# Performance work log

Hardware: AMD Instinct MI355X
Metric: run time of the kernel (lower is better)

The kernel has to match this reference:

```python
import jax, jax.numpy as jnp
import numpy as np

B, CK, CQ, CV, CO, H, W = 4, 256, 256, 256, 64, 24, 24


def setup_inputs() -> dict:
    key = jax.random.key(0)
    ks = jax.random.split(key, 9)
    s = lambda k, shape, fan: jax.random.normal(k, shape, jnp.float32) * (fan ** -0.5)
    return {
        "key": jax.random.normal(ks[0], (B, CK, H, W), jnp.float32),
        "query": jax.random.normal(ks[1], (B, CQ, H, W), jnp.float32),
        "value": jax.random.normal(ks[2], (B, CV, H, W), jnp.float32),
        "Wk": s(ks[3], (CO, CK), CK),   # 1x1 conv weight for key transform
        "bk": jnp.zeros((CO,), jnp.float32),
        "Wq": s(ks[4], (CO, CQ), CQ),   # 1x1 conv weight for query transform
        "bq": jnp.zeros((CO,), jnp.float32),
        "wf": s(ks[5], (CO,), CO),      # channel-flattening 1x1 conv (CO -> 1)
        "bf": jnp.zeros((), jnp.float32),
    }


def reference(key, query, value, Wk, bk, Wq, bq, wf, bf):
    b, _, hq, wq = query.shape
    nk = key.shape[2] * key.shape[3]
    nq = hq * wq
    # 1x1 conv == per-pixel linear; flatten spatial to (B, N, CO)
    k_ = jnp.einsum('bchw,oc->bhwo', key, Wk).reshape(b, nk, -1) + bk
    q_ = jnp.einsum('bchw,oc->bhwo', query, Wq).reshape(b, nq, -1) + bq
    # broadcast add: (B, Nk, 1, CO) + (B, 1, Nq, CO) -> tanh -> reduce channels
    pre = jnp.tanh(k_[:, :, None, :] + q_[:, None, :, :])
    scores = jnp.einsum('bkqc,c->bkq', pre, wf) + bf
    attn = jax.nn.sigmoid(scores)                      # (B, Nk, Nq)
    v_ = value.reshape(b, value.shape[1], nk)          # (B, CV, Nk)
    out = jnp.einsum('bkq,bck->bcq', attn, v_)         # (B, CV, Nq)
    return out.reshape(b, value.shape[1], hq, wq)
```

## Files before the change

kernel.cpp:

```cpp
#include <hip/hip_runtime.h>
#include <hip/hip_bf16.h>

#define BB 4
#define CIN 256
#define CO 64
#define NN 576
#define NKC 18
#define NQT 36

typedef __attribute__((ext_vector_type(8))) short short8;
typedef __attribute__((ext_vector_type(4))) float floatx4;

__device__ __forceinline__ unsigned short f2bf(float f) {
    unsigned int u = __float_as_uint(f);
    unsigned int r = (u + 0x7fffu + ((u >> 16) & 1u)) >> 16;
    return (unsigned short)r;
}

__global__ void __launch_bounds__(256) proj_exp_fused(
    const float* __restrict__ key, const float* __restrict__ query,
    const float* __restrict__ Wk, const float* __restrict__ Wq,
    const float* __restrict__ bk, const float* __restrict__ bq,
    float* __restrict__ ek, float* __restrict__ eq)
{
    int nt16 = blockIdx.x;
    int b    = blockIdx.y;
    int z    = blockIdx.z;
    const float* src  = z ? query : key;
    const float* W    = z ? Wq : Wk;
    const float* bias = z ? bq : bk;
    float*       outp = z ? eq : ek;

    __shared__ float tile[256 * 17];

    int t = threadIdx.x, l = t & 63, w = t >> 6;

    const float* sbase = src + (size_t)b * CIN * NN + (size_t)nt16 * 16;
    #pragma unroll
    for (int i = 0; i < 4; ++i) {
        int f4  = t + i * 256;
        int c   = f4 >> 2;
        int col = (f4 & 3) * 4;
        float4 v = *(const float4*)(sbase + (size_t)c * NN + col);
        float* d = &tile[c * 17 + col];
        d[0] = v.x; d[1] = v.y; d[2] = v.z; d[3] = v.w;
    }
    __syncthreads();

    int nt = w;
    int m  = l & 15;
    int o  = nt * 16 + (l & 15);
    floatx4 acc = {0.f, 0.f, 0.f, 0.f};
    #pragma unroll
    for (int kc = 0; kc < 8; ++kc) {
        int cb = kc * 32 + (l >> 4) * 8;
        short8 a;
        #pragma unroll
        for (int j = 0; j < 8; ++j)
            a[j] = (short)f2bf(tile[(cb + j) * 17 + m]);
        const float4* p = (const float4*)(W + (size_t)o * CIN + cb);
        float4 v0 = p[0], v1 = p[1];
        short8 bfr;
        bfr[0] = (short)f2bf(v0.x); bfr[1] = (short)f2bf(v0.y);
        bfr[2] = (short)f2bf(v0.z); bfr[3] = (short)f2bf(v0.w);
        bfr[4] = (short)f2bf(v1.x); bfr[5] = (short)f2bf(v1.y);
        bfr[6] = (short)f2bf(v1.z); bfr[7] = (short)f2bf(v1.w);
        acc = __builtin_amdgcn_mfma_f32_16x16x32_bf16(a, bfr, acc, 0, 0, 0);
    }

    int n0 = nt16 * 16;
    float bv = bias[o];
    #pragma unroll
    for (int rr = 0; rr < 4; ++rr) {
        int row = (l >> 4) * 4 + rr;
        outp[((size_t)b * NN + n0 + row) * CO + o] = __expf(2.0f * (acc[rr] + bv));
    }
}

__global__ void __launch_bounds__(256, 3) attn_pack_kernel(
    const float* __restrict__ ek, const float* __restrict__ eq,
    const float* __restrict__ wf, const float* __restrict__ bfp,
    unsigned short* __restrict__ Bp)
{
    int b  = blockIdx.z;
    int k0 = blockIdx.y * 32;
    int q0 = blockIdx.x * 64;
    int t  = threadIdx.x;
    int l  = t & 63;
    int w  = __builtin_amdgcn_readfirstlane(t >> 6);

    __shared__ float eqs[64 * 65];
    __shared__ float sc[32 * 65];

    const float4* esrc = (const float4*)(eq + ((size_t)b * NN + q0) * CO);
    #pragma unroll
    for (int i = 0; i < 4; ++i) {
        int f4  = t + i * 256;
        int row = f4 >> 4, c4 = (f4 & 15) * 4;
        float4 v = esrc[f4];
        int a = row * 65 + c4;
        eqs[a + 0] = v.x; eqs[a + 1] = v.y; eqs[a + 2] = v.z; eqs[a + 3] = v.w;
    }

    float4 w2v[16];
    float C = bfp[0];
    const float4* wfp4 = (const float4*)wf;
    #pragma unroll
    for (int i = 0; i < 16; ++i) {
        float4 wv = wfp4[i];
        C += wv.x + wv.y + wv.z + wv.w;
        wv.x *= 2.0f; wv.y *= 2.0f; wv.z *= 2.0f; wv.w *= 2.0f;
        w2v[i] = wv;
    }
    __syncthreads();

    float4 eqv[16];
    #pragma unroll
    for (int i = 0; i < 16; ++i) {
        int a = l * 65 + i * 4;
        eqv[i].x = eqs[a]; eqv[i].y = eqs[a + 1];
        eqv[i].z = eqs[a + 2]; eqv[i].w = eqs[a + 3];
    }

    #pragma unroll 1
    for (int kk = 0; kk < 8; ++kk) {
        int k = k0 + w * 8 + kk;
        const float4* ekr = (const float4*)(ek + ((size_t)b * NN + k) * CO);
        float a0 = 0.f, a1 = 0.f, a2 = 0.f, a3 = 0.f;
        #pragma unroll
        for (int i = 0; i < 16; ++i) {
            float4 k4 = ekr[i];
            float4 e4 = eqv[i];
            float4 w4 = w2v[i];
            a0 = fmaf(w4.x, __builtin_amdgcn_rcpf(fmaf(k4.x, e4.x, 1.0f)), a0);
            a1 = fmaf(w4.y, __builtin_amdgcn_rcpf(fmaf(k4.y, e4.y, 1.0f)), a1);
            a2 = fmaf(w4.z, __builtin_amdgcn_rcpf(fmaf(k4.z, e4.z, 1.0f)), a2);
            a3 = fmaf(w4.w, __builtin_amdgcn_rcpf(fmaf(k4.w, e4.w, 1.0f)), a3);
        }
        float score = C - (a0 + a1) - (a2 + a3);
        float sg = __builtin_amdgcn_rcpf(1.0f + __expf(-score));
        sc[(w * 8 + kk) * 65 + l] = sg;
    }
    __syncthreads();

    int col = w * 16 + (l & 15);
    int row = (l >> 4) * 8;
    uint4 o;
    o.x = (unsigned)f2bf(sc[(row + 0) * 65 + col]) | ((unsigned)f2bf(sc[(row + 1) * 65 + col]) << 16);
    o.y = (unsigned)f2bf(sc[(row + 2) * 65 + col]) | ((unsigned)f2bf(sc[(row + 3) * 65 + col]) << 16);
    o.z = (unsigned)f2bf(sc[(row + 4) * 65 + col]) | ((unsigned)f2bf(sc[(row + 5) * 65 + col]) << 16);
    o.w = (unsigned)f2bf(sc[(row + 6) * 65 + col]) | ((unsigned)f2bf(sc[(row + 7) * 65 + col]) << 16);
    size_t qt = (size_t)blockIdx.x * 4 + w;
    *(uint4*)(Bp + (((size_t)b * NQT + qt) * NKC + blockIdx.y) * 512 + l * 8) = o;
}

__global__ void __launch_bounds__(256) av_mfma_kernel(
    const float* __restrict__ value,
    const unsigned short* __restrict__ Bp,
    float* __restrict__ out)
{
    int b  = blockIdx.z;
    int ct = blockIdx.y;
    int qx = blockIdx.x;
    int t  = threadIdx.x;
    int l  = t & 63;
    int w  = __builtin_amdgcn_readfirstlane(t >> 6);

    floatx4 acc[4] = {{0.f,0.f,0.f,0.f},{0.f,0.f,0.f,0.f},
                      {0.f,0.f,0.f,0.f},{0.f,0.f,0.f,0.f}};

    const float* vb = value + ((size_t)b * CIN + ct * 16 + (l & 15)) * NN + (l >> 4) * 8;
    const unsigned short* bbase = Bp + ((size_t)b * NQT + (size_t)qx * 4) * NKC * 512 + l * 8;

    for (int kc = w; kc < NKC; kc += 4) {
        const float4* p = (const float4*)(vb + kc * 32);
        float4 v0 = p[0], v1 = p[1];
        short8 a;
        a[0] = (short)f2bf(v0.x); a[1] = (short)f2bf(v0.y);
        a[2] = (short)f2bf(v0.z); a[3] = (short)f2bf(v0.w);
        a[4] = (short)f2bf(v1.x); a[5] = (short)f2bf(v1.y);
        a[6] = (short)f2bf(v1.z); a[7] = (short)f2bf(v1.w);
        #pragma unroll
        for (int qt = 0; qt < 4; ++qt) {
            short8 bq = *(const short8*)(bbase + ((size_t)qt * NKC + kc) * 512);
            acc[qt] = __builtin_amdgcn_mfma_f32_16x16x32_bf16(a, bq, acc[qt], 0, 0, 0);
        }
    }

    __shared__ float red[4][64][17];
    #pragma unroll
    for (int qt = 0; qt < 4; ++qt)
        #pragma unroll
        for (int r = 0; r < 4; ++r)
            red[w][l][qt * 4 + r] = acc[qt][r];
    __syncthreads();

    int q = qx * 64 + w * 16 + (l & 15);
    #pragma unroll
    for (int r = 0; r < 4; ++r) {
        float s = red[0][l][w * 4 + r] + red[1][l][w * 4 + r]
                + red[2][l][w * 4 + r] + red[3][l][w * 4 + r];
        int c = ct * 16 + (l >> 4) * 4 + r;
        out[((size_t)b * CIN + c) * NN + q] = s;
    }
}

extern "C" void kernel_launch(void* const* d_in, const int* in_sizes, int n_in,
                              void* d_out, int out_size, void* d_ws, size_t ws_size,
                              hipStream_t stream) {
    const float* key   = (const float*)d_in[0];
    const float* query = (const float*)d_in[1];
    const float* value = (const float*)d_in[2];
    const float* Wk    = (const float*)d_in[3];
    const float* bk    = (const float*)d_in[4];
    const float* Wq    = (const float*)d_in[5];
    const float* bq    = (const float*)d_in[6];
    const float* wf    = (const float*)d_in[7];
    const float* bf    = (const float*)d_in[8];
    float* out = (float*)d_out;

    float* ws = (float*)d_ws;
    float* ek = ws;
    float* eq = ek + (size_t)BB * NN * CO;
    unsigned short* Bp = (unsigned short*)(eq + (size_t)BB * NN * CO);

    dim3 gp(NN / 16, BB, 2);
    proj_exp_fused<<<gp, 256, 0, stream>>>(key, query, Wk, Wq, bk, bq, ek, eq);

    dim3 ga(NN / 64, NN / 32, BB);
    attn_pack_kernel<<<ga, 256, 0, stream>>>(ek, eq, wf, bf, Bp);

    dim3 gm(NN / 64, 16, BB);
    av_mfma_kernel<<<gm, 256, 0, stream>>>(value, Bp, out);
}
```

Before: 102.9 us.

## Fuse all stages into one cooperative kernel with grid syncs and prepack V

Replaces three separate launches with a single cooperative kernel of 648 blocks that runs projection, attention scoring and AV matmul as stages separated by grid.sync, and falls back to separate kernels if the cooperative launch fails. It also adds a stage that converts value to bf16 in MFMA fragment layout alongside the projection, so the AV stage loads packed fragments instead of converting fp32 on the fly. The goal is to remove launch gaps and redundant per-block conversions. The costs are grid-barrier overhead, occupancy limits needed for co-residency, and extra workspace traffic for the packed V.

```diff
diff --git a/kernel.cpp b/kernel.cpp
--- a/kernel.cpp
+++ b/kernel.cpp
@@ -1,5 +1,7 @@
 #include <hip/hip_runtime.h>
-#include <hip/hip_bf16.h>
+#include <hip/hip_cooperative_groups.h>
+
+namespace cg = cooperative_groups;
 
 #define BB 4
 #define CIN 256
@@ -17,23 +19,19 @@
     return (unsigned short)r;
 }
 
-__global__ void __launch_bounds__(256) proj_exp_fused(
+__device__ __forceinline__ void stage_proj(
+    int z, int b, int nt16, int t,
     const float* __restrict__ key, const float* __restrict__ query,
     const float* __restrict__ Wk, const float* __restrict__ Wq,
     const float* __restrict__ bk, const float* __restrict__ bq,
-    float* __restrict__ ek, float* __restrict__ eq)
-{
-    int nt16 = blockIdx.x;
-    int b    = blockIdx.y;
-    int z    = blockIdx.z;
+    float* __restrict__ ek, float* __restrict__ eq,
+    float* tile )
+{
+    int l = t & 63, w = t >> 6;
     const float* src  = z ? query : key;
     const float* W    = z ? Wq : Wk;
     const float* bias = z ? bq : bk;
     float*       outp = z ? eq : ek;
-
-    __shared__ float tile[256 * 17];
-
-    int t = threadIdx.x, l = t & 63, w = t >> 6;
 
     const float* sbase = src + (size_t)b * CIN * NN + (size_t)nt16 * 16;
     #pragma unroll
@@ -47,9 +45,8 @@
     }
     __syncthreads();
 
-    int nt = w;
-    int m  = l & 15;
-    int o  = nt * 16 + (l & 15);
+    int m = l & 15;
+    int o = w * 16 + (l & 15);
     floatx4 acc = {0.f, 0.f, 0.f, 0.f};
     #pragma unroll
     for (int kc = 0; kc < 8; ++kc) {
@@ -77,20 +74,37 @@
     }
 }
 
-__global__ void __launch_bounds__(256, 3) attn_pack_kernel(
+__device__ __forceinline__ void stage_vpack(
+    int funit, int l, const float* __restrict__ value,
+    unsigned short* __restrict__ Vp)
+{
+    int b  = funit / 288;
+    int r  = funit % 288;
+    int ct = r / 18;
+    int kc = r % 18;
+    int c = ct * 16 + (l & 15);
+    int k = kc * 32 + (l >> 4) * 8;
+    const float4* p = (const float4*)(value + ((size_t)b * CIN + c) * NN + k);
+    float4 v0 = p[0], v1 = p[1];
+    uint4 u;
+    u.x = (unsigned)f2bf(v0.x) | ((unsigned)f2bf(v0.y) << 16);
+    u.y = (unsigned)f2bf(v0.z) | ((unsigned)f2bf(v0.w) << 16);
+    u.z = (unsigned)f2bf(v1.x) | ((unsigned)f2bf(v1.y) << 16);
+    u.w = (unsigned)f2bf(v1.z) | ((unsigned)f2bf(v1.w) << 16);
+    *(uint4*)(Vp + (((size_t)b * 16 + ct) * NKC + kc) * 512 + l * 8) = u;
+}
+
+__device__ __forceinline__ void stage_attn(
+    int b, int ky, int qx, int t,
     const float* __restrict__ ek, const float* __restrict__ eq,
     const float* __restrict__ wf, const float* __restrict__ bfp,
-    unsigned short* __restrict__ Bp)
-{
-    int b  = blockIdx.z;
-    int k0 = blockIdx.y * 32;
-    int q0 = blockIdx.x * 64;
-    int t  = threadIdx.x;
+    unsigned short* __restrict__ Bp,
+    float* eqs , float* sc )
+{
+    int k0 = ky * 32;
+    int q0 = qx * 64;
     int l  = t & 63;
     int w  = __builtin_amdgcn_readfirstlane(t >> 6);
-
-    __shared__ float eqs[64 * 65];
-    __shared__ float sc[32 * 65];
 
     const float4* esrc = (const float4*)(eq + ((size_t)b * NN + q0) * CO);
     #pragma unroll
@@ -150,36 +164,27 @@
     o.y = (unsigned)f2bf(sc[(row + 2) * 65 + col]) | ((unsigned)f2bf(sc[(row + 3) * 65 + col]) << 16);
     o.z = (unsigned)f2bf(sc[(row + 4) * 65 + col]) | ((unsigned)f2bf(sc[(row + 5) * 65 + col]) << 16);
     o.w = (unsigned)f2bf(sc[(row + 6) * 65 + col]) | ((unsigned)f2bf(sc[(row + 7) * 65 + col]) << 16);
-    size_t qt = (size_t)blockIdx.x * 4 + w;
-    *(uint4*)(Bp + (((size_t)b * NQT + qt) * NKC + blockIdx.y) * 512 + l * 8) = o;
-}
-
-__global__ void __launch_bounds__(256) av_mfma_kernel(
-    const float* __restrict__ value,
+    size_t qt = (size_t)qx * 4 + w;
+    *(uint4*)(Bp + (((size_t)b * NQT + qt) * NKC + ky) * 512 + l * 8) = o;
+}
+
+__device__ __forceinline__ void stage_av(
+    int b, int ct, int qx, int t,
+    const unsigned short* __restrict__ Vp,
     const unsigned short* __restrict__ Bp,
-    float* __restrict__ out)
-{
-    int b  = blockIdx.z;
-    int ct = blockIdx.y;
-    int qx = blockIdx.x;
-    int t  = threadIdx.x;
-    int l  = t & 63;
-    int w  = __builtin_amdgcn_readfirstlane(t >> 6);
+    float* __restrict__ out, float* red )
+{
+    int l = t & 63;
+    int w = __builtin_amdgcn_readfirstlane(t >> 6);
 
     floatx4 acc[4] = {{0.f,0.f,0.f,0.f},{0.f,0.f,0.f,0.f},
                       {0.f,0.f,0.f,0.f},{0.f,0.f,0.f,0.f}};
 
-    const float* vb = value + ((size_t)b * CIN + ct * 16 + (l & 15)) * NN + (l >> 4) * 8;
+    const unsigned short* abase = Vp + ((size_t)b * 16 + ct) * NKC * 512 + l * 8;
     const unsigned short* bbase = Bp + ((size_t)b * NQT + (size_t)qx * 4) * NKC * 512 + l * 8;
 
     for (int kc = w; kc < NKC; kc += 4) {
-        const float4* p = (const float4*)(vb + kc * 32);
-        float4 v0 = p[0], v1 = p[1];
-        short8 a;
-        a[0] = (short)f2bf(v0.x); a[1] = (short)f2bf(v0.y);
-        a[2] = (short)f2bf(v0.z); a[3] = (short)f2bf(v0.w);
-        a[4] = (short)f2bf(v1.x); a[5] = (short)f2bf(v1.y);
-        a[6] = (short)f2bf(v1.z); a[7] = (short)f2bf(v1.w);
+        short8 a = *(const short8*)(abase + (size_t)kc * 512);
         #pragma unroll
         for (int qt = 0; qt < 4; ++qt) {
             short8 bq = *(const short8*)(bbase + ((size_t)qt * NKC + kc) * 512);
@@ -187,22 +192,94 @@
         }
     }
 
-    __shared__ float red[4][64][17];
     #pragma unroll
     for (int qt = 0; qt < 4; ++qt)
         #pragma unroll
         for (int r = 0; r < 4; ++r)
-            red[w][l][qt * 4 + r] = acc[qt][r];
+            red[(w * 64 + l) * 17 + qt * 4 + r] = acc[qt][r];
     __syncthreads();
 
     int q = qx * 64 + w * 16 + (l & 15);
     #pragma unroll
     for (int r = 0; r < 4; ++r) {
-        float s = red[0][l][w * 4 + r] + red[1][l][w * 4 + r]
-                + red[2][l][w * 4 + r] + red[3][l][w * 4 + r];
+        float s = red[(0 * 64 + l) * 17 + w * 4 + r] + red[(1 * 64 + l) * 17 + w * 4 + r]
+                + red[(2 * 64 + l) * 17 + w * 4 + r] + red[(3 * 64 + l) * 17 + w * 4 + r];
         int c = ct * 16 + (l >> 4) * 4 + r;
         out[((size_t)b * CIN + c) * NN + q] = s;
     }
+}
+
+__global__ void __launch_bounds__(256, 3) mega_fused(
+    const float* __restrict__ key, const float* __restrict__ query,
+    const float* __restrict__ value,
+    const float* __restrict__ Wk, const float* __restrict__ bk,
+    const float* __restrict__ Wq, const float* __restrict__ bq,
+    const float* __restrict__ wf, const float* __restrict__ bfp,
+    float* __restrict__ ek, float* __restrict__ eq,
+    unsigned short* __restrict__ Vp, unsigned short* __restrict__ Bp,
+    float* __restrict__ out)
+{
+    __shared__ float smem[64 * 65 + 32 * 65];
+    cg::grid_group grid = cg::this_grid();
+    int bid = blockIdx.x;
+    int t = threadIdx.x, l = t & 63, w = t >> 6;
+
+    if (bid < 288) {
+        int z = bid / 144, r = bid % 144;
+        int b = r / 36, nt16 = r % 36;
+        stage_proj(z, b, nt16, t, key, query, Wk, Wq, bk, bq, ek, eq, smem);
+    } else if (bid < 576) {
+        stage_vpack((bid - 288) * 4 + w, l, value, Vp);
+    }
+    grid.sync();
+
+    {
+        int b = bid / 162, r = bid % 162;
+        int ky = r / 9, qx = r % 9;
+        stage_attn(b, ky, qx, t, ek, eq, wf, bfp, Bp, smem, smem + 64 * 65);
+    }
+    grid.sync();
+
+    if (bid < 576) {
+        int b = bid / 144, r = bid % 144;
+        int ct = r / 9, qx = r % 9;
+        stage_av(b, ct, qx, t, Vp, Bp, out, smem);
+    }
+}
+
+__global__ void __launch_bounds__(256) proj_kernel(
+    const float* __restrict__ key, const float* __restrict__ query,
+    const float* __restrict__ Wk, const float* __restrict__ Wq,
+    const float* __restrict__ bk, const float* __restrict__ bq,
+    float* __restrict__ ek, float* __restrict__ eq)
+{
+    __shared__ float tile[256 * 17];
+    stage_proj(blockIdx.z, blockIdx.y, blockIdx.x, threadIdx.x,
+               key, query, Wk, Wq, bk, bq, ek, eq, tile);
+}
+
+__global__ void __launch_bounds__(256) vpack_kernel(
+    const float* __restrict__ value, unsigned short* __restrict__ Vp)
+{
+    stage_vpack(blockIdx.x * 4 + (threadIdx.x >> 6), threadIdx.x & 63, value, Vp);
+}
+
+__global__ void __launch_bounds__(256, 3) attn_kernel(
+    const float* __restrict__ ek, const float* __restrict__ eq,
+    const float* __restrict__ wf, const float* __restrict__ bfp,
+    unsigned short* __restrict__ Bp)
+{
+    __shared__ float smem[64 * 65 + 32 * 65];
+    stage_attn(blockIdx.z, blockIdx.y, blockIdx.x, threadIdx.x,
+               ek, eq, wf, bfp, Bp, smem, smem + 64 * 65);
+}
+
+__global__ void __launch_bounds__(256) av_kernel(
+    const unsigned short* __restrict__ Vp,
+    const unsigned short* __restrict__ Bp, float* __restrict__ out)
+{
+    __shared__ float red[4 * 64 * 17];
+    stage_av(blockIdx.z, blockIdx.y, blockIdx.x, threadIdx.x, Vp, Bp, out, red);
 }
 
 extern "C" void kernel_launch(void* const* d_in, const int* in_sizes, int n_in,
@@ -223,13 +300,24 @@
     float* ek = ws;
     float* eq = ek + (size_t)BB * NN * CO;
     unsigned short* Bp = (unsigned short*)(eq + (size_t)BB * NN * CO);
-
-    dim3 gp(NN / 16, BB, 2);
-    proj_exp_fused<<<gp, 256, 0, stream>>>(key, query, Wk, Wq, bk, bq, ek, eq);
-
-    dim3 ga(NN / 64, NN / 32, BB);
-    attn_pack_kernel<<<ga, 256, 0, stream>>>(ek, eq, wf, bf, Bp);
-
-    dim3 gm(NN / 64, 16, BB);
-    av_mfma_kernel<<<gm, 256, 0, stream>>>(value, Bp, out);
-}
+    unsigned short* Vp = Bp + (size_t)BB * NQT * NKC * 512;
+
+    void* args[] = {
+        (void*)&key, (void*)&query, (void*)&value,
+        (void*)&Wk, (void*)&bk, (void*)&Wq, (void*)&bq,
+        (void*)&wf, (void*)&bf,
+        (void*)&ek, (void*)&eq, (void*)&Vp, (void*)&Bp, (void*)&out
+    };
+    hipError_t err = hipLaunchCooperativeKernel(
+        (const void*)mega_fused, dim3(648), dim3(256), args, 0, stream);
+
+    if (err != hipSuccess) {
+        dim3 gp(NN / 16, BB, 2);
+        proj_kernel<<<gp, 256, 0, stream>>>(key, query, Wk, Wq, bk, bq, ek, eq);
+        vpack_kernel<<<288, 256, 0, stream>>>(value, Vp);
+        dim3 ga(NN / 64, NN / 32, BB);
+        attn_kernel<<<ga, 256, 0, stream>>>(ek, eq, wf, bf, Bp);
+        dim3 gm(NN / 64, 16, BB);
+        av_kernel<<<gm, 256, 0, stream>>>(Vp, Bp, out);
+    }
+}
```

New measurement: 299.7 us. 191% more time.
